# Optimization experiments

Measured on AMD Instinct MI355X. Metric: run time of the kernel, lower is better.

The kernel has to match this reference:

```python
import jax, jax.numpy as jnp
import numpy as np

N_E = 8192
E_DIM = 256
BETA = 0.25


def setup_inputs() -> dict:
    key = jax.random.key(0)
    k1, k2 = jax.random.split(key)
    z = jax.random.normal(k1, (4, 256, 16, 16, 16), dtype=jnp.float32)
    weight = jax.random.normal(k2, (N_E, E_DIM), dtype=jnp.float32)
    return {"z": z, "weight": weight}


def reference(z, weight):
    # b c l h w -> b l h w c
    zc = jnp.transpose(z, (0, 2, 3, 4, 1))
    zf = zc.reshape(-1, E_DIM)  # [N, D]
    n = zf.shape[0]

    # squared euclidean distances to all codes: [N, n_e]
    d = (jnp.sum(zf * zf, axis=1, keepdims=True)
         + jnp.sum(weight * weight, axis=1)
         - 2.0 * jnp.einsum('bd,nd->bn', zf, weight))
    idx = jnp.argmin(d, axis=1)  # [N] int

    z_q = weight[idx].reshape(zc.shape)  # codebook gather

    # histogram of code usage (equivalent to one-hot mean, without the NxK one-hot)
    counts = jnp.zeros((N_E,), dtype=zf.dtype).at[idx].add(1.0)
    avg_probs = counts / jnp.asarray(n, zf.dtype)
    perplexity = jnp.exp(-jnp.sum(avg_probs * jnp.log(avg_probs + 1e-10)))
    unique = jnp.sum(counts > 0).astype(jnp.int32)

    # commitment loss (z_q detached) + straight-through estimator
    loss = BETA * jnp.mean((jax.lax.stop_gradient(z_q) - zc) ** 2)
    z_q_st = zc + jax.lax.stop_gradient(z_q - zc)

    # b l h w c -> b c l h w
    z_q_out = jnp.transpose(z_q_st, (0, 4, 1, 2, 3))
    return z_q_out, loss, perplexity, unique, idx
```

## Files before the change

### kernel.cpp

```cpp
#include <hip/hip_runtime.h>

#define NQ     16384
#define EDIM   256
#define NE     8192
#define LHW    4096
#define BETA   0.25f

#define WS_WSQ    0
#define WS_CNT    32768
#define WS_LOSS   65536
#define WS_IDX    65792
#define WS_BEST   131328
#define WS_APACK  2359552
#define WS_BPACK  10748160
#define WS_S1     14942464
#define WS_NEED   23331072

typedef __attribute__((ext_vector_type(8))) short bf16x8;
typedef __attribute__((ext_vector_type(4))) float f32x4;

__device__ __forceinline__ unsigned f32_sortable(float f) {
    unsigned b = __float_as_uint(f);
    return b ^ ((unsigned)((int)b >> 31) | 0x80000000u);
}
__device__ __forceinline__ unsigned short bf16_rn(float f) {
    unsigned u = __float_as_uint(f);
    return (unsigned short)((u + 0x7FFFu + ((u >> 16) & 1u)) >> 16);
}

__global__ __launch_bounds__(1024) void pack_all(const float* __restrict__ w,
                                                 const float* __restrict__ z,
                                                 float* __restrict__ wsq,
                                                 unsigned* __restrict__ Bp32,
                                                 unsigned* __restrict__ Ap32,
                                                 unsigned* __restrict__ counts,
                                                 float* __restrict__ loss,
                                                 unsigned* __restrict__ done) {
    __shared__ unsigned lds[64 * 129];
    int tid = threadIdx.x;
    if (blockIdx.x < 512) {
        int wave = tid >> 6, lane = tid & 63;
        int row = blockIdx.x * 16 + wave;
        if (blockIdx.x < 8) {
            counts[blockIdx.x * 1024 + tid] = 0u;
            if (blockIdx.x == 0 && tid == 0) { loss[0] = 0.f; done[0] = 0u; }
        }
        float4 v = *(const float4*)(w + (size_t)row * EDIM + lane * 4);
        double s = (double)v.x * v.x + (double)v.y * v.y +
                   (double)v.z * v.z + (double)v.w * v.w;
        unsigned p0 = (unsigned)bf16_rn(v.x) | ((unsigned)bf16_rn(v.y) << 16);
        unsigned p1 = (unsigned)bf16_rn(v.z) | ((unsigned)bf16_rn(v.w) << 16);
        *(uint2*)(Bp32 + (size_t)row * 128 + lane * 2) = make_uint2(p0, p1);
        #pragma unroll
        for (int off = 32; off; off >>= 1) s += __shfl_xor(s, off, 64);
        if (lane == 0) wsq[row] = (float)s;
    } else {
        int bz = blockIdx.x - 512;
        int tn = tid & 63, tc = tid >> 6;
        int n0 = bz * 64;
        int n = n0 + tn;
        int b = n >> 12, lhw = n & 4095;
        #pragma unroll
        for (int cc = 0; cc < 16; cc += 2) {
            int d = tc * 16 + cc;
            float v0 = z[((size_t)b * EDIM + d) * LHW + lhw];
            float v1 = z[((size_t)b * EDIM + d + 1) * LHW + lhw];
            lds[tn * 129 + (d >> 1)] =
                (unsigned)bf16_rn(v0) | ((unsigned)bf16_rn(v1) << 16);
        }
        __syncthreads();
        #pragma unroll
        for (int p = 0; p < 8; ++p) {
            int flat = p * 1024 + tid;
            int row = flat >> 7, c = flat & 127;
            Ap32[(size_t)(n0 + row) * 128 + c] = lds[row * 129 + c];
        }
    }
}

__global__ __launch_bounds__(256) void wsq_kernel(const float* __restrict__ w,
                                                  float* __restrict__ wsq) {
    int wave = threadIdx.x >> 6, lane = threadIdx.x & 63;
    int row = blockIdx.x * 4 + wave;
    float4 v = *(const float4*)(w + (size_t)row * EDIM + lane * 4);
    double s = (double)v.x * v.x + (double)v.y * v.y +
               (double)v.z * v.z + (double)v.w * v.w;
    #pragma unroll
    for (int off = 32; off; off >>= 1) s += __shfl_xor(s, off, 64);
    if (lane == 0) wsq[row] = (float)s;
}

__global__ __launch_bounds__(256, 3) void dist_mfma(const unsigned short* __restrict__ Ap,
                                                    const unsigned short* __restrict__ Bp,
                                                    const float* __restrict__ wsq,
                                                    unsigned* __restrict__ s1) {
    __shared__ __align__(16) unsigned short lds_b[2][128 * 64];
    int tid = threadIdx.x, lane = tid & 63, w = tid >> 6;
    int x = blockIdx.x, nt = blockIdx.y;
    int quad = lane >> 4, col = lane & 15;
    int rsel = lane >> 3, seg = lane & 7;

    const unsigned short* arow = Ap + (size_t)(nt * 128 + w * 32 + col) * 256;
    const unsigned short* Bbase = Bp + (size_t)(x * 128) * 256;

    f32x4 acc[2][8];
    #pragma unroll
    for (int i = 0; i < 2; ++i)
        #pragma unroll
        for (int j = 0; j < 8; ++j) acc[i][j] = (f32x4){0.f, 0.f, 0.f, 0.f};

    auto stage_chunk = [&](int kc, int bsel) {
        int k0s = kc * 64;
        #pragma unroll
        for (int p = 0; p < 4; ++p) {
            int c = w * 4 + p;
            const unsigned short* gb =
                Bbase + (size_t)(c * 8 + rsel) * 256 + k0s + ((seg ^ (rsel & 7)) * 8);
            __builtin_amdgcn_global_load_lds(
                (const __attribute__((address_space(1))) void*)gb,
                (__attribute__((address_space(3))) void*)(&lds_b[bsel][c * 512]),
                16, 0, 0);
        }
    };

    stage_chunk(0, 0);

    #pragma unroll
    for (int kcc = 0; kcc < 4; ++kcc) {
        int k0 = kcc * 64;
        int cur = kcc & 1;
        bf16x8 af[2][2];
        #pragma unroll
        for (int i = 0; i < 2; ++i)
            #pragma unroll
            for (int h = 0; h < 2; ++h)
                af[i][h] = *(const bf16x8*)(arow + i * 16 * 256 + k0 + h * 32 + quad * 8);
        asm volatile("" ::: "memory");
        if (kcc < 3) {
            stage_chunk(kcc + 1, cur ^ 1);
            asm volatile("s_waitcnt vmcnt(8)" ::: "memory");
        } else {
            asm volatile("s_waitcnt vmcnt(4)" ::: "memory");
        }
        __builtin_amdgcn_s_barrier();
        asm volatile("" ::: "memory");
        __builtin_amdgcn_s_setprio(1);
        #pragma unroll
        for (int h = 0; h < 2; ++h) {
            bf16x8 bf[8];
            #pragma unroll
            for (int j = 0; j < 8; ++j)
                bf[j] = *(const bf16x8*)(&lds_b[cur][(j * 16 + col) * 64 +
                                         (((h * 4 + quad) ^ (col & 7)) * 8)]);
            #pragma unroll
            for (int i = 0; i < 2; ++i)
                #pragma unroll
                for (int j = 0; j < 8; ++j)
                    acc[i][j] = __builtin_amdgcn_mfma_f32_16x16x32_bf16(
                        af[i][h], bf[j], acc[i][j], 0, 0, 0);
        }
        __builtin_amdgcn_s_setprio(0);
        asm volatile("" ::: "memory");
        if (kcc < 3) {
            __builtin_amdgcn_s_barrier();
            asm volatile("" ::: "memory");
        }
    }

    unsigned m1[2][4], m2[2][4];
    #pragma unroll
    for (int i = 0; i < 2; ++i)
        #pragma unroll
        for (int r = 0; r < 4; ++r) { m1[i][r] = 0xFFFFFFFFu; m2[i][r] = 0xFFFFFFFFu; }
    #pragma unroll
    for (int j = 0; j < 8; ++j) {
        int e = x * 128 + j * 16 + col;
        unsigned jc = (unsigned)(j * 16 + col);
        float wq_off = wsq[e] + 4096.0f;
        #pragma unroll
        for (int i = 0; i < 2; ++i)
            #pragma unroll
            for (int r = 0; r < 4; ++r) {
                float d = fmaf(-2.0f, acc[i][j][r], wq_off);
                unsigned k = (__float_as_uint(d) & 0xFFFFFF80u) | jc;
                unsigned mx = (m1[i][r] > k) ? m1[i][r] : k;
                m1[i][r] = (m1[i][r] < k) ? m1[i][r] : k;
                m2[i][r] = (m2[i][r] < mx) ? m2[i][r] : mx;
            }
    }
    #pragma unroll
    for (int i = 0; i < 2; ++i)
        #pragma unroll
        for (int r = 0; r < 4; ++r) {
            unsigned a1 = m1[i][r], a2 = m2[i][r];
            #pragma unroll
            for (int off = 1; off < 16; off <<= 1) {
                unsigned b1 = __shfl_xor(a1, off, 64);
                unsigned b2 = __shfl_xor(a2, off, 64);
                unsigned lo1 = a1 < b1 ? a1 : b1;
                unsigned hi1 = a1 < b1 ? b1 : a1;
                unsigned lo2 = a2 < b2 ? a2 : b2;
                a1 = lo1;
                a2 = hi1 < lo2 ? hi1 : lo2;
            }
            if (col == 0) {
                int q = nt * 128 + w * 32 + i * 16 + quad * 4 + r;
                size_t o = (size_t)x * (NQ * 2) + (size_t)q * 2;
                s1[o] = a1; s1[o + 1] = a2;
            }
        }
}

__global__ __launch_bounds__(256, 2) void dist_fp32(const float* __restrict__ z,
                                                    const float* __restrict__ w,
                                                    const float* __restrict__ wsq,
                                                    unsigned long long* __restrict__ best) {
    __shared__ float lds_a[32 * 128];
    __shared__ float lds_b[32 * 132];
    int tid = threadIdx.x;
    int tx = tid & 15, ty = tid >> 4;
    int n0 = blockIdx.y * 128;
    int bb_ = n0 >> 12, lhw0 = n0 & 4095;
    const float* zb = z + (size_t)bb_ * (EDIM * LHW) + lhw0;
    int ebase = blockIdx.x * 2048;
    unsigned long long runmin[8];
    #pragma unroll
    for (int i = 0; i < 8; ++i) runmin[i] = ~0ull;
    float acc[64];
    for (int et = 0; et < 16; ++et) {
        int e0 = ebase + et * 128;
        #pragma unroll
        for (int i = 0; i < 64; ++i) acc[i] = 0.f;
        for (int kc = 0; kc < 8; ++kc) {
            int k0 = kc * 32;
            #pragma unroll
            for (int p = 0; p < 4; ++p) {
                int f = p * 256 + tid;
                int kk = f >> 5, nn4 = f & 31;
                float4 v = *(const float4*)(zb + (size_t)(k0 + kk) * LHW + nn4 * 4);
                *((float4*)(lds_a + kk * 128 + nn4 * 4)) = v;
            }
            #pragma unroll
            for (int p = 0; p < 4; ++p) {
                int f = p * 256 + tid;
                int ee = f >> 3, kk4 = f & 7;
                float4 v = *(const float4*)(w + (size_t)(e0 + ee) * EDIM + k0 + kk4 * 4);
                lds_b[(kk4 * 4 + 0) * 132 + ee] = v.x;
                lds_b[(kk4 * 4 + 1) * 132 + ee] = v.y;
                lds_b[(kk4 * 4 + 2) * 132 + ee] = v.z;
                lds_b[(kk4 * 4 + 3) * 132 + ee] = v.w;
            }
            __syncthreads();
            #pragma unroll
            for (int k = 0; k < 32; ++k) {
                float a[8], bv[8];
                *(float4*)(a)      = *(float4*)(lds_a + k * 128 + ty * 8);
                *(float4*)(a + 4)  = *(float4*)(lds_a + k * 128 + ty * 8 + 4);
                *(float4*)(bv)     = *(float4*)(lds_b + k * 132 + tx * 8);
                *(float4*)(bv + 4) = *(float4*)(lds_b + k * 132 + tx * 8 + 4);
                #pragma unroll
                for (int i = 0; i < 8; ++i)
                    #pragma unroll
                    for (int j = 0; j < 8; ++j)
                        acc[i * 8 + j] = fmaf(a[i], bv[j], acc[i * 8 + j]);
            }
            __syncthreads();
        }
        #pragma unroll
        for (int i = 0; i < 8; ++i) {
            unsigned long long m = runmin[i];
            #pragma unroll
            for (int j = 0; j < 8; ++j) {
                int e = e0 + tx * 8 + j;
                float d = wsq[e] - 2.0f * acc[i * 8 + j];
                unsigned long long key =
                    ((unsigned long long)f32_sortable(d) << 32) | (unsigned)e;
                m = (m < key) ? m : key;
            }
            runmin[i] = m;
        }
    }
    #pragma unroll
    for (int i = 0; i < 8; ++i) {
        unsigned long long kk = runmin[i];
        #pragma unroll
        for (int off = 8; off >= 1; off >>= 1) {
            unsigned long long o = __shfl_xor(kk, off, 16);
            kk = (kk < o) ? kk : o;
        }
        if (tx == 0) atomicMin(&best[n0 + ty * 8 + i], kk);
    }
}

__global__ __launch_bounds__(256) void extract_idx(const unsigned long long* __restrict__ best,
                                                   unsigned* __restrict__ idxarr) {
    int n = blockIdx.x * 256 + threadIdx.x;
    idxarr[n] = (unsigned)(best[n] & 0xFFFFFFFFull) & (NE - 1);
}

__global__ __launch_bounds__(1024) void gather_kernel(const float* __restrict__ z,
                                                      const float* __restrict__ w,
                                                      const float* __restrict__ wsq,
                                                      const unsigned* __restrict__ s1,
                                                      const unsigned* __restrict__ idxarr,
                                                      unsigned* __restrict__ counts,
                                                      float* __restrict__ loss,
                                                      unsigned* __restrict__ done,
                                                      float* __restrict__ out,
                                                      float* __restrict__ out_idx,
                                                      float* __restrict__ out_scalars) {
    __shared__ float zt[64 * 272];
    __shared__ float wl[64 * 257];
    __shared__ int idx_s[64];
    __shared__ float lsum[16];
    __shared__ int usum[16];
    __shared__ unsigned lastflag;
    int tid = threadIdx.x, lane = tid & 63, wv = tid >> 6;
    int n0 = blockIdx.x * 64;
    int bb_ = n0 >> 12, lhw0 = n0 & 4095;
    const float* zb = z + (size_t)bb_ * (EDIM * LHW) + lhw0;

    {
        int l = tid & 63, dg = tid >> 6;
        #pragma unroll
        for (int i = 0; i < 16; ++i) {
            int d = dg * 16 + i;
            zt[l * 272 + d] = zb[(size_t)d * LHW + l];
        }
    }
    __syncthreads();

    if (s1 != nullptr) {
        #pragma unroll
        for (int jq = 0; jq < 4; ++jq) {
            int ql = wv * 4 + jq;
            int q = n0 + ql;
            uint2 kk2 = *(const uint2*)(s1 + ((size_t)lane * NQ + q) * 2);
            unsigned long long a1 = ((unsigned long long)(kk2.x >> 7) << 13)
                                  | (unsigned)(lane * 128 + (kk2.x & 127u));
            unsigned long long a2 = ((unsigned long long)(kk2.y >> 7) << 13)
                                  | (unsigned)(lane * 128 + (kk2.y & 127u));
            #pragma unroll
            for (int off = 1; off < 8; off <<= 1) {
                unsigned long long b1 = __shfl_xor(a1, off, 64);
                unsigned long long b2 = __shfl_xor(a2, off, 64);
                unsigned long long lo1 = a1 < b1 ? a1 : b1;
                unsigned long long hi1 = a1 < b1 ? b1 : a1;
                unsigned long long lo2 = a2 < b2 ? a2 : b2;
                a1 = lo1;
                a2 = hi1 < lo2 ? hi1 : lo2;
            }
            float4 zv4 = *(const float4*)(&zt[ql * 272 + lane * 4]);
            unsigned long long bestk = ~0ull;
            #pragma unroll
            for (int c = 0; c < 16; ++c) {
                int src = (c >> 1) * 8;
                unsigned long long kc = (c & 1) ? __shfl(a2, src, 64)
                                                : __shfl(a1, src, 64);
                unsigned e = (unsigned)(kc & (unsigned long long)(NE - 1));
                float4 wv4 = *(const float4*)(w + (size_t)e * EDIM + lane * 4);
                float p = zv4.x * wv4.x + zv4.y * wv4.y +
                          zv4.z * wv4.z + zv4.w * wv4.w;
                #pragma unroll
                for (int off = 32; off; off >>= 1) p += __shfl_xor(p, off, 64);
                float d = wsq[e] - 2.0f * p;
                unsigned long long key =
                    ((unsigned long long)f32_sortable(d) << 32) | e;
                if (key < bestk) bestk = key;
            }
            if (lane == 0) {
                int idx = (int)(bestk & 0xFFFFFFFFull) & (NE - 1);
                idx_s[ql] = idx;
                out_idx[q] = (float)idx;
                atomicAdd(&counts[idx], 1u);
            }
        }
    } else {
        if (tid < 64) {
            int idx = (int)(idxarr[n0 + tid] & (NE - 1));
            idx_s[tid] = idx;
            out_idx[n0 + tid] = (float)idx;
            atomicAdd(&counts[idx], 1u);
        }
    }
    __syncthreads();

    {
        int r0 = tid >> 8, cl = tid & 255;
        #pragma unroll
        for (int i = 0; i < 16; ++i)
            wl[(r0 + i * 4) * 257 + cl] = w[(size_t)idx_s[r0 + i * 4] * EDIM + cl];
    }
    __syncthreads();

    int tn = tid & 63, tc = tid >> 6;
    size_t ob = (size_t)bb_ * (EDIM * LHW) + lhw0 + tn;
    float accl = 0.f;
    #pragma unroll
    for (int cc = 0; cc < 16; ++cc) {
        int c = tc * 16 + cc;
        float wv_ = wl[tn * 257 + c];
        float zv = zt[tn * 272 + c];
        float diff = wv_ - zv;
        out[ob + (size_t)c * LHW] = zv + diff;
        accl += diff * diff;
    }
    #pragma unroll
    for (int off = 32; off; off >>= 1) accl += __shfl_xor(accl, off, 64);
    if (lane == 0) lsum[wv] = accl;
    __syncthreads();
    if (tid < 16) {
        float v = lsum[tid];
        v += __shfl_xor(v, 8, 16);
        v += __shfl_xor(v, 4, 16);
        v += __shfl_xor(v, 2, 16);
        v += __shfl_xor(v, 1, 16);
        if (tid == 0) atomicAdd(loss, v);
    }

    __syncthreads();
    if (tid == 0) {
        __threadfence();
        lastflag = (atomicAdd(done, 1u) == (unsigned)(NQ / 64 - 1));
    }
    __syncthreads();
    if (lastflag) {
        __threadfence();
        float s = 0.f;
        int uniq = 0;
        for (int i = tid; i < NE; i += 1024) {
            unsigned c = counts[i];
            if (c > 0) {
                float p = (float)c * (1.0f / (float)NQ);
                s += p * logf(p + 1e-10f);
                uniq++;
            }
        }
        #pragma unroll
        for (int off = 32; off; off >>= 1) {
            s += __shfl_xor(s, off, 64);
            uniq += __shfl_xor(uniq, off, 64);
        }
        if (lane == 0) { lsum[wv] = s; usum[wv] = uniq; }
        __syncthreads();
        if (tid == 0) {
            float st = 0.f;
            int ut = 0;
            #pragma unroll
            for (int i = 0; i < 16; ++i) { st += lsum[i]; ut += usum[i]; }
            out_scalars[0] = BETA * loss[0] * (1.0f / (float)(NQ * EDIM));
            out_scalars[1] = expf(-st);
            out_scalars[2] = (float)ut;
        }
    }
}

extern "C" void kernel_launch(void* const* d_in, const int* in_sizes, int n_in,
                              void* d_out, int out_size, void* d_ws, size_t ws_size,
                              hipStream_t stream) {
    const float* z = (const float*)d_in[0];
    const float* w = (const float*)d_in[1];
    float* out = (float*)d_out;
    char* ws = (char*)d_ws;
    float* wsq = (float*)(ws + WS_WSQ);
    unsigned* counts = (unsigned*)(ws + WS_CNT);
    float* loss = (float*)(ws + WS_LOSS);
    unsigned* done = (unsigned*)(ws + WS_LOSS + 4);
    unsigned* idxarr = (unsigned*)(ws + WS_IDX);
    unsigned long long* best = (unsigned long long*)(ws + WS_BEST);
    unsigned* Ap = (unsigned*)(ws + WS_APACK);
    unsigned* Bp = (unsigned*)(ws + WS_BPACK);
    unsigned* s1 = (unsigned*)(ws + WS_S1);

    int idx_off = out_size - NQ;
    int scal_off = idx_off - 3;
    float* out_idx = out + idx_off;
    float* out_scalars = out + scal_off;

    if (ws_size >= (size_t)WS_NEED) {
        pack_all<<<768, 1024, 0, stream>>>(w, z, wsq, Bp, Ap, counts, loss, done);
        dist_mfma<<<dim3(64, 128), 256, 0, stream>>>((const unsigned short*)Ap,
                                                     (const unsigned short*)Bp, wsq, s1);
        gather_kernel<<<NQ / 64, 1024, 0, stream>>>(z, w, wsq, s1, idxarr, counts,
                                                    loss, done, out, out_idx, out_scalars);
    } else {
        hipMemsetAsync(counts, 0, NE * sizeof(unsigned), stream);
        hipMemsetAsync(loss, 0, 8, stream);
        wsq_kernel<<<NE / 4, 256, 0, stream>>>(w, wsq);
        hipMemsetAsync(best, 0xFF, NQ * sizeof(unsigned long long), stream);
        dist_fp32<<<dim3(4, 128), 256, 0, stream>>>(z, w, wsq, best);
        extract_idx<<<NQ / 256, 256, 0, stream>>>(best, idxarr);
        gather_kernel<<<NQ / 64, 1024, 0, stream>>>(z, w, wsq, nullptr, idxarr, counts,
                                                    loss, done, out, out_idx, out_scalars);
    }
}
```

Before: 220.2 us.

## Swizzle distance blocks across XCDs and vectorize z transpose loads

Remaps the dist_mfma block index so that each group of consecutive hardware-dispatched blocks, which round-robin across the XCDs, lands on one XCD with contiguous query/code tiles. The aim is better L2 reuse of the packed A and B operands. pack_all and gather_kernel now read z with float4 loads and transpose through LDS, with bf16 packing done per element in a 16-bit LDS array. gather_kernel is also halved to 32 queries per 512-thread block, which doubles the grid and may change occupancy. The tradeoff is extra scattered LDS stores and more atomic and done-counter traffic from the larger number of blocks.

New measurement: 233.0 us. 1.06x slower.

```diff
diff --git a/kernel.cpp b/kernel.cpp
--- a/kernel.cpp
+++ b/kernel.cpp
@@ -36,7 +36,7 @@
                                                  unsigned* __restrict__ counts,
                                                  float* __restrict__ loss,
                                                  unsigned* __restrict__ done) {
-    __shared__ unsigned lds[64 * 129];
+    __shared__ unsigned short lds16[64 * 258];
     int tid = threadIdx.x;
     if (blockIdx.x < 512) {
         int wave = tid >> 6, lane = tid & 63;
@@ -56,24 +56,26 @@
         if (lane == 0) wsq[row] = (float)s;
     } else {
         int bz = blockIdx.x - 512;
-        int tn = tid & 63, tc = tid >> 6;
         int n0 = bz * 64;
-        int n = n0 + tn;
-        int b = n >> 12, lhw = n & 4095;
-        #pragma unroll
-        for (int cc = 0; cc < 16; cc += 2) {
-            int d = tc * 16 + cc;
-            float v0 = z[((size_t)b * EDIM + d) * LHW + lhw];
-            float v1 = z[((size_t)b * EDIM + d + 1) * LHW + lhw];
-            lds[tn * 129 + (d >> 1)] =
-                (unsigned)bf16_rn(v0) | ((unsigned)bf16_rn(v1) << 16);
+        int b = n0 >> 12, lhwb = n0 & 4095;
+        const float* zb = z + (size_t)b * (EDIM * LHW) + lhwb;
+        int s = tid & 15, dg = tid >> 4;
+        #pragma unroll
+        for (int r = 0; r < 4; ++r) {
+            int d = r * 64 + dg;
+            float4 v = *(const float4*)(zb + (size_t)d * LHW + s * 4);
+            lds16[(s * 4 + 0) * 258 + d] = bf16_rn(v.x);
+            lds16[(s * 4 + 1) * 258 + d] = bf16_rn(v.y);
+            lds16[(s * 4 + 2) * 258 + d] = bf16_rn(v.z);
+            lds16[(s * 4 + 3) * 258 + d] = bf16_rn(v.w);
         }
         __syncthreads();
         #pragma unroll
         for (int p = 0; p < 8; ++p) {
             int flat = p * 1024 + tid;
             int row = flat >> 7, c = flat & 127;
-            Ap32[(size_t)(n0 + row) * 128 + c] = lds[row * 129 + c];
+            Ap32[(size_t)(n0 + row) * 128 + c] =
+                *(const unsigned*)(&lds16[row * 258 + 2 * c]);
         }
     }
 }
@@ -96,7 +98,9 @@
                                                     unsigned* __restrict__ s1) {
     __shared__ __align__(16) unsigned short lds_b[2][128 * 64];
     int tid = threadIdx.x, lane = tid & 63, w = tid >> 6;
-    int x = blockIdx.x, nt = blockIdx.y;
+    int fl = blockIdx.y * 64 + blockIdx.x;
+    int nf = (fl & 7) * 1024 + (fl >> 3);
+    int x = nf & 63, nt = nf >> 6;
     int quad = lane >> 4, col = lane & 15;
     int rsel = lane >> 3, seg = lane & 7;
 
@@ -298,34 +302,38 @@
     idxarr[n] = (unsigned)(best[n] & 0xFFFFFFFFull) & (NE - 1);
 }
 
-__global__ __launch_bounds__(1024) void gather_kernel(const float* __restrict__ z,
-                                                      const float* __restrict__ w,
-                                                      const float* __restrict__ wsq,
-                                                      const unsigned* __restrict__ s1,
-                                                      const unsigned* __restrict__ idxarr,
-                                                      unsigned* __restrict__ counts,
-                                                      float* __restrict__ loss,
-                                                      unsigned* __restrict__ done,
-                                                      float* __restrict__ out,
-                                                      float* __restrict__ out_idx,
-                                                      float* __restrict__ out_scalars) {
-    __shared__ float zt[64 * 272];
-    __shared__ float wl[64 * 257];
-    __shared__ int idx_s[64];
-    __shared__ float lsum[16];
-    __shared__ int usum[16];
+__global__ __launch_bounds__(512) void gather_kernel(const float* __restrict__ z,
+                                                     const float* __restrict__ w,
+                                                     const float* __restrict__ wsq,
+                                                     const unsigned* __restrict__ s1,
+                                                     const unsigned* __restrict__ idxarr,
+                                                     unsigned* __restrict__ counts,
+                                                     float* __restrict__ loss,
+                                                     unsigned* __restrict__ done,
+                                                     float* __restrict__ out,
+                                                     float* __restrict__ out_idx,
+                                                     float* __restrict__ out_scalars) {
+    __shared__ float zt[32 * 276];
+    __shared__ float wl[32 * 257];
+    __shared__ int idx_s[32];
+    __shared__ float lsum[8];
+    __shared__ int usum[8];
     __shared__ unsigned lastflag;
     int tid = threadIdx.x, lane = tid & 63, wv = tid >> 6;
-    int n0 = blockIdx.x * 64;
+    int n0 = blockIdx.x * 32;
     int bb_ = n0 >> 12, lhw0 = n0 & 4095;
     const float* zb = z + (size_t)bb_ * (EDIM * LHW) + lhw0;
 
     {
-        int l = tid & 63, dg = tid >> 6;
-        #pragma unroll
-        for (int i = 0; i < 16; ++i) {
-            int d = dg * 16 + i;
-            zt[l * 272 + d] = zb[(size_t)d * LHW + l];
+        int s = tid & 7, dg = tid >> 3;
+        #pragma unroll
+        for (int r = 0; r < 4; ++r) {
+            int d = r * 64 + dg;
+            float4 v = *(const float4*)(zb + (size_t)d * LHW + s * 4);
+            zt[(s * 4 + 0) * 276 + d] = v.x;
+            zt[(s * 4 + 1) * 276 + d] = v.y;
+            zt[(s * 4 + 2) * 276 + d] = v.z;
+            zt[(s * 4 + 3) * 276 + d] = v.w;
         }
     }
     __syncthreads();
@@ -350,7 +358,7 @@
                 a1 = lo1;
                 a2 = hi1 < lo2 ? hi1 : lo2;
             }
-            float4 zv4 = *(const float4*)(&zt[ql * 272 + lane * 4]);
+            float4 zv4 = *(const float4*)(&zt[ql * 276 + lane * 4]);
             unsigned long long bestk = ~0ull;
             #pragma unroll
             for (int c = 0; c < 16; ++c) {
@@ -376,7 +384,7 @@
             }
         }
     } else {
-        if (tid < 64) {
+        if (tid < 32) {
             int idx = (int)(idxarr[n0 + tid] & (NE - 1));
             idx_s[tid] = idx;
             out_idx[n0 + tid] = (float)idx;
@@ -389,18 +397,18 @@
         int r0 = tid >> 8, cl = tid & 255;
         #pragma unroll
         for (int i = 0; i < 16; ++i)
-            wl[(r0 + i * 4) * 257 + cl] = w[(size_t)idx_s[r0 + i * 4] * EDIM + cl];
+            wl[(r0 + i * 2) * 257 + cl] = w[(size_t)idx_s[r0 + i * 2] * EDIM + cl];
     }
     __syncthreads();
 
-    int tn = tid & 63, tc = tid >> 6;
+    int tn = tid & 31, tc = tid >> 5;
     size_t ob = (size_t)bb_ * (EDIM * LHW) + lhw0 + tn;
     float accl = 0.f;
     #pragma unroll
     for (int cc = 0; cc < 16; ++cc) {
         int c = tc * 16 + cc;
         float wv_ = wl[tn * 257 + c];
-        float zv = zt[tn * 272 + c];
+        float zv = zt[tn * 276 + c];
         float diff = wv_ - zv;
         out[ob + (size_t)c * LHW] = zv + diff;
         accl += diff * diff;
@@ -409,26 +417,25 @@
     for (int off = 32; off; off >>= 1) accl += __shfl_xor(accl, off, 64);
     if (lane == 0) lsum[wv] = accl;
     __syncthreads();
-    if (tid < 16) {
+    if (tid < 8) {
         float v = lsum[tid];
-        v += __shfl_xor(v, 8, 16);
-        v += __shfl_xor(v, 4, 16);
-        v += __shfl_xor(v, 2, 16);
-        v += __shfl_xor(v, 1, 16);
+        v += __shfl_xor(v, 4, 8);
+        v += __shfl_xor(v, 2, 8);
+        v += __shfl_xor(v, 1, 8);
         if (tid == 0) atomicAdd(loss, v);
     }
 
     __syncthreads();
     if (tid == 0) {
         __threadfence();
-        lastflag = (atomicAdd(done, 1u) == (unsigned)(NQ / 64 - 1));
+        lastflag = (atomicAdd(done, 1u) == (unsigned)(NQ / 32 - 1));
     }
     __syncthreads();
     if (lastflag) {
         __threadfence();
         float s = 0.f;
         int uniq = 0;
-        for (int i = tid; i < NE; i += 1024) {
+        for (int i = tid; i < NE; i += 512) {
             unsigned c = counts[i];
             if (c > 0) {
                 float p = (float)c * (1.0f / (float)NQ);
@@ -447,7 +454,7 @@
             float st = 0.f;
             int ut = 0;
             #pragma unroll
-            for (int i = 0; i < 16; ++i) { st += lsum[i]; ut += usum[i]; }
+            for (int i = 0; i < 8; ++i) { st += lsum[i]; ut += usum[i]; }
             out_scalars[0] = BETA * loss[0] * (1.0f / (float)(NQ * EDIM));
             out_scalars[1] = expf(-st);
             out_scalars[2] = (float)ut;
@@ -481,8 +488,8 @@
         pack_all<<<768, 1024, 0, stream>>>(w, z, wsq, Bp, Ap, counts, loss, done);
         dist_mfma<<<dim3(64, 128), 256, 0, stream>>>((const unsigned short*)Ap,
                                                      (const unsigned short*)Bp, wsq, s1);
-        gather_kernel<<<NQ / 64, 1024, 0, stream>>>(z, w, wsq, s1, idxarr, counts,
-                                                    loss, done, out, out_idx, out_scalars);
+        gather_kernel<<<NQ / 32, 512, 0, stream>>>(z, w, wsq, s1, idxarr, counts,
+                                                   loss, done, out, out_idx, out_scalars);
     } else {
         hipMemsetAsync(counts, 0, NE * sizeof(unsigned), stream);
         hipMemsetAsync(loss, 0, 8, stream);
@@ -490,7 +497,7 @@
         hipMemsetAsync(best, 0xFF, NQ * sizeof(unsigned long long), stream);
         dist_fp32<<<dim3(4, 128), 256, 0, stream>>>(z, w, wsq, best);
         extract_idx<<<NQ / 256, 256, 0, stream>>>(best, idxarr);
-        gather_kernel<<<NQ / 64, 1024, 0, stream>>>(z, w, wsq, nullptr, idxarr, counts,
-                                                    loss, done, out, out_idx, out_scalars);
-    }
-}
+        gather_kernel<<<NQ / 32, 512, 0, stream>>>(z, w, wsq, nullptr, idxarr, counts,
+                                                   loss, done, out, out_idx, out_scalars);
+    }
+}
```
